# Performance work log

Hardware: AMD Instinct MI355X
Metric: run time of the kernel (lower is better)

Reference implementation:

```python
import jax, jax.numpy as jnp
import numpy as np

BINS = 10


def setup_inputs() -> dict:
    key = jax.random.key(0)
    k1, k2 = jax.random.split(key)
    N, C = 4194304, 16
    inputs = jax.random.normal(k1, (N, C), dtype=jnp.float32)
    target = jax.random.randint(k2, (N,), 0, 2, dtype=jnp.int64)
    return {"inputs": inputs, "target": target}


def reference(inputs, target):
    N = inputs.shape[0]
    edges = jnp.arange(BINS + 1, dtype=inputs.dtype) / BINS  # [0, 0.1, ..., 1.0]

    # p_t = softmax(inputs)[i, target_i]
    logp = jax.nn.log_softmax(inputs, axis=1)
    p_t = jnp.take_along_axis(jnp.exp(logp), target[:, None], axis=1)[:, 0]

    # gradient norm g = |p_t - target| (detached in the original)
    g = jnp.abs(jax.lax.stop_gradient(p_t) - target.astype(inputs.dtype))

    # bin index: matches (g >= edges[i]) & (g < edges[i+1]); clip handles g == 1.0
    bin_idx = jnp.clip(jnp.searchsorted(edges, g, side="right") - 1, 0, BINS - 1)

    # per-bin counts via one scatter-add (replaces the per-bin CPU loop)
    counts = jax.ops.segment_sum(jnp.ones_like(g), bin_idx, num_segments=BINS)
    counts = jnp.maximum(counts, 1.0)  # occupied bins always have count >= 1

    # weights[i] = (N / bins) / num_in_bin(i)
    weights = (N / BINS) / counts[bin_idx]

    # weighted cross entropy, summed
    nll = -jnp.take_along_axis(logp, target[:, None], axis=1)[:, 0]
    return jnp.sum(nll * weights)
```

## Files before the change

kernel.cpp:

```cpp
#include <hip/hip_runtime.h>

#define BINS 10
#define PAD 11
#define GRID 1024
#define BLOCK 256

__global__ __launch_bounds__(BLOCK) void ghm_main(const float* __restrict__ x,
                                                  const int* __restrict__ tgt,
                                                  float* __restrict__ p_sum,
                                                  unsigned int* __restrict__ p_cnt,
                                                  int n_rows) {
    __shared__ float s_sum[BLOCK * PAD];
    __shared__ unsigned int s_cnt[BLOCK * PAD];

    const int t = threadIdx.x;
    #pragma unroll
    for (int b = 0; b < BINS; ++b) { s_sum[t * PAD + b] = 0.0f; s_cnt[t * PAD + b] = 0u; }

    const int gid = blockIdx.x * BLOCK + t;
    const int nthreads = GRID * BLOCK;
    const float4* __restrict__ xv = (const float4*)x;

    const float edges[BINS] = {0.1f, 0.2f, 0.3f, 0.4f, 0.5f,
                               0.6f, 0.7f, 0.8f, 0.9f, 1.0f};

    for (int r = gid; r < n_rows; r += nthreads) {
        const float4 v0 = xv[(size_t)r * 4 + 0];
        const float4 v1 = xv[(size_t)r * 4 + 1];
        const float4 v2 = xv[(size_t)r * 4 + 2];
        const float4 v3 = xv[(size_t)r * 4 + 3];
        const int tg = tgt[r];

        float m = fmaxf(fmaxf(fmaxf(v0.x, v0.y), fmaxf(v0.z, v0.w)),
                        fmaxf(fmaxf(v1.x, v1.y), fmaxf(v1.z, v1.w)));
        m = fmaxf(m, fmaxf(fmaxf(fmaxf(v2.x, v2.y), fmaxf(v2.z, v2.w)),
                           fmaxf(fmaxf(v3.x, v3.y), fmaxf(v3.z, v3.w))));

        float s = expf(v0.x - m) + expf(v0.y - m) + expf(v0.z - m) + expf(v0.w - m)
                + expf(v1.x - m) + expf(v1.y - m) + expf(v1.z - m) + expf(v1.w - m)
                + expf(v2.x - m) + expf(v2.y - m) + expf(v2.z - m) + expf(v2.w - m)
                + expf(v3.x - m) + expf(v3.y - m) + expf(v3.z - m) + expf(v3.w - m);

        const float4 vs = (tg < 8) ? ((tg < 4) ? v0 : v1) : ((tg < 12) ? v2 : v3);
        const int c = tg & 3;
        const float xt = (c < 2) ? ((c == 0) ? vs.x : vs.y) : ((c == 2) ? vs.z : vs.w);

        const float logp = xt - m - logf(s);
        const float g = fabsf(expf(logp) - (float)tg);

        int b = 0;
        #pragma unroll
        for (int k = 0; k < BINS; ++k) b += (g >= edges[k]) ? 1 : 0;
        if (b > BINS - 1) b = BINS - 1;

        s_sum[t * PAD + b] += -logp;
        s_cnt[t * PAD + b] += 1u;
    }
    __syncthreads();

    for (int off = BLOCK / 2; off > 0; off >>= 1) {
        if (t < off) {
            #pragma unroll
            for (int b = 0; b < BINS; ++b) {
                s_sum[t * PAD + b] += s_sum[(t + off) * PAD + b];
                s_cnt[t * PAD + b] += s_cnt[(t + off) * PAD + b];
            }
        }
        __syncthreads();
    }

    if (t < BINS) {
        p_sum[t * GRID + blockIdx.x] = s_sum[t];
        p_cnt[t * GRID + blockIdx.x] = s_cnt[t];
    }
}

__global__ void ghm_final(const float* __restrict__ p_sum,
                          const unsigned int* __restrict__ p_cnt,
                          float* __restrict__ out, int n_rows) {
    const int lane = threadIdx.x;
    double total = 0.0;
    for (int b = 0; b < BINS; ++b) {
        double s = 0.0;
        unsigned long long c = 0;
        for (int k = lane; k < GRID; k += 64) {
            s += (double)p_sum[b * GRID + k];
            c += (unsigned long long)p_cnt[b * GRID + k];
        }
        #pragma unroll
        for (int off = 32; off > 0; off >>= 1) {
            s += __shfl_xor(s, off);
            c += __shfl_xor(c, off);
        }
        double cd = (double)c;
        if (cd < 1.0) cd = 1.0;
        total += s / cd;
    }
    if (lane == 0) out[0] = (float)(total * ((double)n_rows / (double)BINS));
}

extern "C" void kernel_launch(void* const* d_in, const int* in_sizes, int n_in,
                              void* d_out, int out_size, void* d_ws, size_t ws_size,
                              hipStream_t stream) {
    const float* x = (const float*)d_in[0];
    const int* tgt = (const int*)d_in[1];
    const int n_rows = in_sizes[1];

    float* p_sum = (float*)d_ws;
    unsigned int* p_cnt = (unsigned int*)((char*)d_ws + BINS * GRID * sizeof(float));

    ghm_main<<<GRID, BLOCK, 0, stream>>>(x, tgt, p_sum, p_cnt, n_rows);
    ghm_final<<<1, 64, 0, stream>>>(p_sum, p_cnt, (float*)d_out, n_rows);
}
```

Before: 420.8 us.

## Use register histograms, wave shuffles, nontemporal loads and fast softmax math

Result: slower. 456.2 us (+8.4%).

```diff
diff --git a/kernel.cpp b/kernel.cpp
--- a/kernel.cpp
+++ b/kernel.cpp
@@ -1,77 +1,85 @@
 #include <hip/hip_runtime.h>
 
 #define BINS 10
-#define PAD 11
-#define GRID 1024
+#define GRID 2048
 #define BLOCK 256
+#define NWAVES (BLOCK / 64)
+
+typedef float vfloat4 __attribute__((ext_vector_type(4)));
 
 __global__ __launch_bounds__(BLOCK) void ghm_main(const float* __restrict__ x,
                                                   const int* __restrict__ tgt,
                                                   float* __restrict__ p_sum,
                                                   unsigned int* __restrict__ p_cnt,
                                                   int n_rows) {
-    __shared__ float s_sum[BLOCK * PAD];
-    __shared__ unsigned int s_cnt[BLOCK * PAD];
+    float h_sum[BINS];
+    unsigned int h_cnt[BINS];
+    #pragma unroll
+    for (int b = 0; b < BINS; ++b) { h_sum[b] = 0.0f; h_cnt[b] = 0u; }
 
-    const int t = threadIdx.x;
-    #pragma unroll
-    for (int b = 0; b < BINS; ++b) { s_sum[t * PAD + b] = 0.0f; s_cnt[t * PAD + b] = 0u; }
-
-    const int gid = blockIdx.x * BLOCK + t;
-    const int nthreads = GRID * BLOCK;
-    const float4* __restrict__ xv = (const float4*)x;
+    const int gid = blockIdx.x * BLOCK + threadIdx.x;
+    const int stride = GRID * BLOCK;
+    const vfloat4* __restrict__ xv = (const vfloat4*)x;
 
     const float edges[BINS] = {0.1f, 0.2f, 0.3f, 0.4f, 0.5f,
                                0.6f, 0.7f, 0.8f, 0.9f, 1.0f};
 
-    for (int r = gid; r < n_rows; r += nthreads) {
-        const float4 v0 = xv[(size_t)r * 4 + 0];
-        const float4 v1 = xv[(size_t)r * 4 + 1];
-        const float4 v2 = xv[(size_t)r * 4 + 2];
-        const float4 v3 = xv[(size_t)r * 4 + 3];
+    for (int r = gid; r < n_rows; r += stride) {
+        const vfloat4 v0 = __builtin_nontemporal_load(&xv[(size_t)r * 4 + 0]);
+        const vfloat4 v1 = __builtin_nontemporal_load(&xv[(size_t)r * 4 + 1]);
+        const vfloat4 v2 = __builtin_nontemporal_load(&xv[(size_t)r * 4 + 2]);
+        const vfloat4 v3 = __builtin_nontemporal_load(&xv[(size_t)r * 4 + 3]);
         const int tg = tgt[r];
 
-        float m = fmaxf(fmaxf(fmaxf(v0.x, v0.y), fmaxf(v0.z, v0.w)),
-                        fmaxf(fmaxf(v1.x, v1.y), fmaxf(v1.z, v1.w)));
-        m = fmaxf(m, fmaxf(fmaxf(fmaxf(v2.x, v2.y), fmaxf(v2.z, v2.w)),
-                           fmaxf(fmaxf(v3.x, v3.y), fmaxf(v3.z, v3.w))));
-
-        float s = expf(v0.x - m) + expf(v0.y - m) + expf(v0.z - m) + expf(v0.w - m)
-                + expf(v1.x - m) + expf(v1.y - m) + expf(v1.z - m) + expf(v1.w - m)
-                + expf(v2.x - m) + expf(v2.y - m) + expf(v2.z - m) + expf(v2.w - m)
-                + expf(v3.x - m) + expf(v3.y - m) + expf(v3.z - m) + expf(v3.w - m);
-
-        const float4 vs = (tg < 8) ? ((tg < 4) ? v0 : v1) : ((tg < 12) ? v2 : v3);
+        const vfloat4 vs = (tg < 8) ? ((tg < 4) ? v0 : v1) : ((tg < 12) ? v2 : v3);
         const int c = tg & 3;
         const float xt = (c < 2) ? ((c == 0) ? vs.x : vs.y) : ((c == 2) ? vs.z : vs.w);
 
-        const float logp = xt - m - logf(s);
-        const float g = fabsf(expf(logp) - (float)tg);
+        const float s =
+            __expf(v0.x - xt) + __expf(v0.y - xt) + __expf(v0.z - xt) + __expf(v0.w - xt) +
+            __expf(v1.x - xt) + __expf(v1.y - xt) + __expf(v1.z - xt) + __expf(v1.w - xt) +
+            __expf(v2.x - xt) + __expf(v2.y - xt) + __expf(v2.z - xt) + __expf(v2.w - xt) +
+            __expf(v3.x - xt) + __expf(v3.y - xt) + __expf(v3.z - xt) + __expf(v3.w - xt);
+
+        const float nll = __logf(s);
+        const float p = 1.0f / s;
+        const float g = fabsf(p - (float)tg);
 
         int b = 0;
         #pragma unroll
         for (int k = 0; k < BINS; ++k) b += (g >= edges[k]) ? 1 : 0;
-        if (b > BINS - 1) b = BINS - 1;
+        b = (b > BINS - 1) ? (BINS - 1) : b;
 
-        s_sum[t * PAD + b] += -logp;
-        s_cnt[t * PAD + b] += 1u;
+        #pragma unroll
+        for (int k = 0; k < BINS; ++k) {
+            if (b == k) { h_sum[k] += nll; h_cnt[k] += 1u; }
+        }
+    }
+
+    __shared__ float ls[NWAVES * BINS];
+    __shared__ unsigned int lc[NWAVES * BINS];
+    const int lane = threadIdx.x & 63;
+    const int wv = threadIdx.x >> 6;
+    #pragma unroll
+    for (int b = 0; b < BINS; ++b) {
+        float s = h_sum[b];
+        unsigned int cn = h_cnt[b];
+        #pragma unroll
+        for (int off = 32; off > 0; off >>= 1) {
+            s += __shfl_xor(s, off);
+            cn += __shfl_xor(cn, off);
+        }
+        if (lane == 0) { ls[wv * BINS + b] = s; lc[wv * BINS + b] = cn; }
     }
     __syncthreads();
 
-    for (int off = BLOCK / 2; off > 0; off >>= 1) {
-        if (t < off) {
-            #pragma unroll
-            for (int b = 0; b < BINS; ++b) {
-                s_sum[t * PAD + b] += s_sum[(t + off) * PAD + b];
-                s_cnt[t * PAD + b] += s_cnt[(t + off) * PAD + b];
-            }
-        }
-        __syncthreads();
-    }
-
-    if (t < BINS) {
-        p_sum[t * GRID + blockIdx.x] = s_sum[t];
-        p_cnt[t * GRID + blockIdx.x] = s_cnt[t];
+    if (threadIdx.x < BINS) {
+        float s = 0.0f;
+        unsigned int cn = 0u;
+        #pragma unroll
+        for (int w = 0; w < NWAVES; ++w) { s += ls[w * BINS + threadIdx.x]; cn += lc[w * BINS + threadIdx.x]; }
+        p_sum[threadIdx.x * GRID + blockIdx.x] = s;
+        p_cnt[threadIdx.x * GRID + blockIdx.x] = cn;
     }
 }
 
```
